# Optimization experiments

Hardware: AMD Instinct MI355X
Metric: run time of the kernel (lower is better)

Reference implementation:

```python
import jax, jax.numpy as jnp
import numpy as np

B, P, NB, WN, CI, CO = 4, 20000, 9, 17, 64, 128

def setup_inputs() -> dict:
    key = jax.random.key(0)
    k0, k1, k2, k3 = jax.random.split(key, 4)
    in_pc = jax.random.normal(k0, (B, P, CI), dtype=jnp.float32)
    raw_w_weights = jax.random.normal(k1, (P, NB, WN), dtype=jnp.float32) * 0.1
    # padded/missing neighbors use id == P, which indexes the zero-pad row and is masked
    neighbor_ids = jax.random.randint(k2, (P, NB), 0, P + 1)
    weights = jax.random.normal(k3, (WN, CO * CI), dtype=jnp.float32)
    bias = jnp.zeros((P, CO), dtype=jnp.float32)
    return {"in_pc": in_pc, "raw_w_weights": raw_w_weights, "weights": weights,
            "bias": bias, "neighbor_ids": neighbor_ids}

def reference(in_pc, raw_w_weights, weights, bias, neighbor_ids):
    b, p, ci = in_pc.shape
    wn = weights.shape[0]
    co = bias.shape[-1]
    # pc_mask: 1 for real points, 0 for the pad row (id == in_pn)
    nb_mask = (neighbor_ids < p).astype(in_pc.dtype)          # [p, nb]
    w_weights = raw_w_weights * nb_mask[:, :, None]           # [p, nb, wn]
    in_pc_pad = jnp.concatenate(
        [in_pc, jnp.zeros((b, 1, ci), dtype=in_pc.dtype)], axis=1)  # [b, p+1, ci]
    in_neighbors = in_pc_pad[:, neighbor_ids]                 # [b, p, nb, ci] gather
    # weighted fuse over neighbors into wn basis slots
    fuse = jnp.einsum('pnm,bpni->bpmi', w_weights, in_neighbors)   # [b, p, wn, ci]
    Wm = weights.reshape(wn, co, ci)
    # per-basis conv then sum-reduce over wn (b_max_pool=False), fused into one einsum
    out_pc = jnp.einsum('moi,bpmi->bpo', Wm, fuse) + bias      # [b, p, co]
    # is_final_layer=False -> ELU; residual_rate=0 -> no residual branch
    return jax.nn.elu(out_pc)
```

## Files before the change

kernel.cpp:

```cpp
#include <hip/hip_runtime.h>
#include <stdint.h>

#define B_   4
#define P_   20000
#define NB_  9
#define WN_  17
#define CI_  64
#define CO_  128
#define PTS  32
#define NBLK (P_ / PTS)

typedef __fp16 f16x8 __attribute__((ext_vector_type(8)));
typedef __fp16 h2    __attribute__((ext_vector_type(2)));
typedef float  f32x16 __attribute__((ext_vector_type(16)));

union H2U { h2 h; uint32_t u; };
union F8U { f16x8 v; h2 h[4]; uint4 u; };

__device__ __forceinline__ int b_idx(int co, int oloc) {
    int slot = (co & 1) | (((oloc ^ ((co >> 1) & 3)) & 3) << 1);
    return (co >> 1) * 64 + slot * 8;
}

__global__ void prep_wm(const float* __restrict__ w, ushort* __restrict__ wsb) {
    int i = blockIdx.x * 256 + threadIdx.x;
    int m  = i >> 10;
    int r  = i & 1023;
    int p  = r >> 9;
    int rr = r & 511;
    int co = rr >> 2, oloc = rr & 3;
    const float* src = w + (size_t)m * (CO_ * CI_) + co * CI_ + (p * 4 + oloc) * 8;
    float4 v0 = *(const float4*)(src);
    float4 v1 = *(const float4*)(src + 4);
    F8U h;
    h.h[0] = __builtin_amdgcn_cvt_pkrtz(v0.x, v0.y);
    h.h[1] = __builtin_amdgcn_cvt_pkrtz(v0.z, v0.w);
    h.h[2] = __builtin_amdgcn_cvt_pkrtz(v1.x, v1.y);
    h.h[3] = __builtin_amdgcn_cvt_pkrtz(v1.z, v1.w);
    *(uint4*)&wsb[(m * 2 + p) * 4096 + b_idx(co, oloc)] = h.u;
}

template <bool PRE>
__global__ __launch_bounds__(256, 2)
void lasm_fused(const float* __restrict__ in_pc,
                const float* __restrict__ raw_w,
                const float* __restrict__ weights,
                const float* __restrict__ bias,
                const int*   __restrict__ nbr,
                const ushort* __restrict__ wsb,
                float*       __restrict__ out)
{
    __shared__ __align__(16) int      s_nid[PTS * NB_];
    __shared__ __align__(16) uint32_t s_w2[WN_ * NB_ * 33];
    __shared__ __align__(16) ushort   s_b[2][4096];

    const int tid  = threadIdx.x;
    const int lane = tid & 63;
    const int w    = tid >> 6;
    const int arow = lane & 31;
    const int q    = lane >> 5;
    const int p0   = blockIdx.x * PTS;

    for (int t = tid; t < PTS * NB_; t += 256) s_nid[t] = nbr[p0 * NB_ + t];
    for (int idx = tid; idx < PTS * NB_ * WN_; idx += 256) {
        int pl  = idx / (NB_ * WN_);
        int rem = idx % (NB_ * WN_);
        int n   = rem / WN_;
        int m   = rem % WN_;
        float wf = raw_w[(size_t)p0 * NB_ * WN_ + idx];
        H2U c; c.h = __builtin_amdgcn_cvt_pkrtz(wf, wf);
        s_w2[(m * NB_ + n) * 33 + pl] = c.u;
    }
    __syncthreads();

    f32x16 acc[4];
    #pragma unroll
    for (int c = 0; c < 4; ++c)
        #pragma unroll
        for (int j = 0; j < 16; ++j) acc[c][j] = 0.f;

    const size_t binpc = (size_t)w * P_ * CI_;

    auto stage_b = [&](int pass, int m, int buf) {
        if (PRE) {
            #pragma unroll
            for (int j = 0; j < 2; ++j) {
                int flat = j * 256 + tid;
                uint4 v = *(const uint4*)&wsb[(size_t)(m * 2 + pass) * 4096 + flat * 8];
                *(uint4*)&s_b[buf][flat * 8] = v;
            }
        } else {
            #pragma unroll
            for (int j = 0; j < 2; ++j) {
                int flat = j * 256 + tid;
                int co = flat >> 2, oloc = flat & 3;
                const float* src = weights + (size_t)m * (CO_ * CI_) + co * CI_ + (pass * 4 + oloc) * 8;
                float4 v0 = *(const float4*)(src);
                float4 v1 = *(const float4*)(src + 4);
                F8U h;
                h.h[0] = __builtin_amdgcn_cvt_pkrtz(v0.x, v0.y);
                h.h[1] = __builtin_amdgcn_cvt_pkrtz(v0.z, v0.w);
                h.h[2] = __builtin_amdgcn_cvt_pkrtz(v1.x, v1.y);
                h.h[3] = __builtin_amdgcn_cvt_pkrtz(v1.z, v1.w);
                *(uint4*)&s_b[buf][b_idx(co, oloc)] = h.u;
            }
        }
    };

    for (int pass = 0; pass < 2; ++pass) {
        h2 x[NB_][8];
        const int ch0 = pass * 32 + q * 8;
        #pragma unroll
        for (int n = 0; n < NB_; ++n) {
            uint32_t nid = (uint32_t)s_nid[arow * NB_ + n];
            if (nid < (uint32_t)P_) {
                const float* src = in_pc + binpc + (size_t)nid * CI_ + ch0;
                float4 a0 = *(const float4*)(src);
                float4 a1 = *(const float4*)(src + 4);
                float4 b0 = *(const float4*)(src + 16);
                float4 b1 = *(const float4*)(src + 20);
                x[n][0] = __builtin_amdgcn_cvt_pkrtz(a0.x, a0.y);
                x[n][1] = __builtin_amdgcn_cvt_pkrtz(a0.z, a0.w);
                x[n][2] = __builtin_amdgcn_cvt_pkrtz(a1.x, a1.y);
                x[n][3] = __builtin_amdgcn_cvt_pkrtz(a1.z, a1.w);
                x[n][4] = __builtin_amdgcn_cvt_pkrtz(b0.x, b0.y);
                x[n][5] = __builtin_amdgcn_cvt_pkrtz(b0.z, b0.w);
                x[n][6] = __builtin_amdgcn_cvt_pkrtz(b1.x, b1.y);
                x[n][7] = __builtin_amdgcn_cvt_pkrtz(b1.z, b1.w);
            } else {
                h2 z = {(__fp16)0.f, (__fp16)0.f};
                #pragma unroll
                for (int j = 0; j < 8; ++j) x[n][j] = z;
            }
        }

        stage_b(pass, 0, 0);
        __syncthreads();

        int cur = 0;
        for (int m = 0; m < WN_; ++m) {
            int nxt = cur ^ 1;
            if (m + 1 < WN_) stage_b(pass, m + 1, nxt);

            H2U wc[9];
            #pragma unroll
            for (int n = 0; n < NB_; ++n) wc[n].u = s_w2[(m * NB_ + n) * 33 + arow];

            F8U f[2];
            #pragma unroll
            for (int kk = 0; kk < 2; ++kk) {
                #pragma unroll
                for (int r4 = 0; r4 < 4; ++r4) {
                    h2 c = {(__fp16)0.f, (__fp16)0.f};
                    #pragma unroll
                    for (int n = 0; n < NB_; ++n) c += wc[n].h * x[n][kk * 4 + r4];
                    f[kk].h[r4] = c;
                }
            }

            #pragma unroll
            for (int kk = 0; kk < 2; ++kk) {
                int oloc = kk * 2 + q;
                #pragma unroll
                for (int c = 0; c < 4; ++c) {
                    int bco = c * 32 + arow;
                    f16x8 bf = *(const f16x8*)&s_b[cur][b_idx(bco, oloc)];
                    acc[c] = __builtin_amdgcn_mfma_f32_32x32x16_f16(f[kk].v, bf, acc[c], 0, 0, 0);
                }
            }
            __syncthreads();
            cur = nxt;
        }
    }

    #pragma unroll
    for (int c = 0; c < 4; ++c) {
        int col = c * 32 + arow;
        #pragma unroll
        for (int v = 0; v < 16; ++v) {
            int lr = (v & 3) + 8 * (v >> 2) + 4 * q;
            int p  = p0 + lr;
            float val = acc[c][v] + bias[(size_t)p * CO_ + col];
            val = (val > 0.f) ? val : (__expf(val) - 1.f);
            out[((size_t)w * P_ + p) * CO_ + col] = val;
        }
    }
}

extern "C" void kernel_launch(void* const* d_in, const int* in_sizes, int n_in,
                              void* d_out, int out_size, void* d_ws, size_t ws_size,
                              hipStream_t stream) {
    const float* in_pc   = (const float*)d_in[0];
    const float* raw_w   = (const float*)d_in[1];
    const float* weights = (const float*)d_in[2];
    const float* bias    = (const float*)d_in[3];
    const int*   nbr     = (const int*)  d_in[4];
    float* out = (float*)d_out;

    const size_t need = (size_t)WN_ * 2 * 4096 * sizeof(ushort);
    if (d_ws != nullptr && ws_size >= need) {
        ushort* wsb = (ushort*)d_ws;
        prep_wm<<<dim3(WN_ * 2 * 512 / 256), dim3(256), 0, stream>>>(weights, wsb);
        lasm_fused<true><<<dim3(NBLK), dim3(256), 0, stream>>>(
            in_pc, raw_w, weights, bias, nbr, wsb, out);
    } else {
        lasm_fused<false><<<dim3(NBLK), dim3(256), 0, stream>>>(
            in_pc, raw_w, weights, bias, nbr, nullptr, out);
    }
}
```

Baseline: 171.3 us.

## Repartition block work across batch and channel halves, load weights directly from global

Halves the points per block and reassigns waves so each wave covers two batches by 16 points for half of the output channels, cutting the accumulator count. The shared-memory double-buffered weight staging and its per-basis barriers are removed; each lane now loads its weight fragments from global (L2) into registers, prefetching one step ahead. The weight prep layout is changed to match, occupancy hint raised to 3 blocks per SM, and output uses nontemporal stores. In exchange, weight fragments are fetched redundantly per wave from cache, and the blend of gathered neighbors is now recomputed by both channel-half waves.

Measured after the change: 164.1 us. -4.2%, faster.

```diff
diff --git a/kernel.cpp b/kernel.cpp
--- a/kernel.cpp
+++ b/kernel.cpp
@@ -7,7 +7,7 @@
 #define WN_  17
 #define CI_  64
 #define CO_  128
-#define PTS  32
+#define PTS  16
 #define NBLK (P_ / PTS)
 
 typedef __fp16 f16x8 __attribute__((ext_vector_type(8)));
@@ -17,18 +17,12 @@
 union H2U { h2 h; uint32_t u; };
 union F8U { f16x8 v; h2 h[4]; uint4 u; };
 
-__device__ __forceinline__ int b_idx(int co, int oloc) {
-    int slot = (co & 1) | (((oloc ^ ((co >> 1) & 3)) & 3) << 1);
-    return (co >> 1) * 64 + slot * 8;
-}
-
 __global__ void prep_wm(const float* __restrict__ w, ushort* __restrict__ wsb) {
     int i = blockIdx.x * 256 + threadIdx.x;
-    int m  = i >> 10;
-    int r  = i & 1023;
-    int p  = r >> 9;
-    int rr = r & 511;
-    int co = rr >> 2, oloc = rr & 3;
+    int m2p  = i >> 9;
+    int r    = i & 511;
+    int oloc = r >> 7, co = r & 127;
+    int m = m2p >> 1, p = m2p & 1;
     const float* src = w + (size_t)m * (CO_ * CI_) + co * CI_ + (p * 4 + oloc) * 8;
     float4 v0 = *(const float4*)(src);
     float4 v1 = *(const float4*)(src + 4);
@@ -37,11 +31,11 @@
     h.h[1] = __builtin_amdgcn_cvt_pkrtz(v0.z, v0.w);
     h.h[2] = __builtin_amdgcn_cvt_pkrtz(v1.x, v1.y);
     h.h[3] = __builtin_amdgcn_cvt_pkrtz(v1.z, v1.w);
-    *(uint4*)&wsb[(m * 2 + p) * 4096 + b_idx(co, oloc)] = h.u;
+    *(uint4*)&wsb[(size_t)((m2p * 4 + oloc) * 128 + co) * 8] = h.u;
 }
 
 template <bool PRE>
-__global__ __launch_bounds__(256, 2)
+__global__ __launch_bounds__(256, 3)
 void lasm_fused(const float* __restrict__ in_pc,
                 const float* __restrict__ raw_w,
                 const float* __restrict__ weights,
@@ -51,59 +45,57 @@
                 float*       __restrict__ out)
 {
     __shared__ __align__(16) int      s_nid[PTS * NB_];
-    __shared__ __align__(16) uint32_t s_w2[WN_ * NB_ * 33];
-    __shared__ __align__(16) ushort   s_b[2][4096];
+    __shared__ __align__(16) uint32_t s_w2[WN_ * NB_ * 17];
 
     const int tid  = threadIdx.x;
     const int lane = tid & 63;
-    const int w    = tid >> 6;
+    const int wv   = tid >> 6;
     const int arow = lane & 31;
     const int q    = lane >> 5;
+    const int mt   = wv >> 1;
+    const int ch   = wv & 1;
     const int p0   = blockIdx.x * PTS;
 
-    for (int t = tid; t < PTS * NB_; t += 256) s_nid[t] = nbr[p0 * NB_ + t];
+    if (tid < PTS * NB_) s_nid[tid] = nbr[p0 * NB_ + tid];
     for (int idx = tid; idx < PTS * NB_ * WN_; idx += 256) {
-        int pl  = idx / (NB_ * WN_);
+        int pl2 = idx / (NB_ * WN_);
         int rem = idx % (NB_ * WN_);
         int n   = rem / WN_;
         int m   = rem % WN_;
         float wf = raw_w[(size_t)p0 * NB_ * WN_ + idx];
         H2U c; c.h = __builtin_amdgcn_cvt_pkrtz(wf, wf);
-        s_w2[(m * NB_ + n) * 33 + pl] = c.u;
+        s_w2[(m * NB_ + n) * 17 + pl2] = c.u;
     }
     __syncthreads();
 
-    f32x16 acc[4];
+    f32x16 acc[2];
     #pragma unroll
-    for (int c = 0; c < 4; ++c)
+    for (int c = 0; c < 2; ++c)
         #pragma unroll
         for (int j = 0; j < 16; ++j) acc[c][j] = 0.f;
 
-    const size_t binpc = (size_t)w * P_ * CI_;
+    const int brow = mt * 2 + (arow >> 4);
+    const int pl   = arow & 15;
+    const size_t binpc = (size_t)brow * P_ * CI_;
 
-    auto stage_b = [&](int pass, int m, int buf) {
+    auto load_b = [&](int m, int pass, int kk, int c) -> f16x8 {
+        int oloc = kk * 2 + q;
         if (PRE) {
-            #pragma unroll
-            for (int j = 0; j < 2; ++j) {
-                int flat = j * 256 + tid;
-                uint4 v = *(const uint4*)&wsb[(size_t)(m * 2 + pass) * 4096 + flat * 8];
-                *(uint4*)&s_b[buf][flat * 8] = v;
-            }
+            F8U r;
+            r.u = *(const uint4*)&wsb[(size_t)(((m * 2 + pass) * 4 + oloc) * 128
+                                               + ch * 64 + c * 32 + arow) * 8];
+            return r.v;
         } else {
-            #pragma unroll
-            for (int j = 0; j < 2; ++j) {
-                int flat = j * 256 + tid;
-                int co = flat >> 2, oloc = flat & 3;
-                const float* src = weights + (size_t)m * (CO_ * CI_) + co * CI_ + (pass * 4 + oloc) * 8;
-                float4 v0 = *(const float4*)(src);
-                float4 v1 = *(const float4*)(src + 4);
-                F8U h;
-                h.h[0] = __builtin_amdgcn_cvt_pkrtz(v0.x, v0.y);
-                h.h[1] = __builtin_amdgcn_cvt_pkrtz(v0.z, v0.w);
-                h.h[2] = __builtin_amdgcn_cvt_pkrtz(v1.x, v1.y);
-                h.h[3] = __builtin_amdgcn_cvt_pkrtz(v1.z, v1.w);
-                *(uint4*)&s_b[buf][b_idx(co, oloc)] = h.u;
-            }
+            const float* s = weights + (size_t)m * (CO_ * CI_)
+                           + (ch * 64 + c * 32 + arow) * CI_ + (pass * 4 + oloc) * 8;
+            float4 v0 = *(const float4*)(s);
+            float4 v1 = *(const float4*)(s + 4);
+            F8U r;
+            r.h[0] = __builtin_amdgcn_cvt_pkrtz(v0.x, v0.y);
+            r.h[1] = __builtin_amdgcn_cvt_pkrtz(v0.z, v0.w);
+            r.h[2] = __builtin_amdgcn_cvt_pkrtz(v1.x, v1.y);
+            r.h[3] = __builtin_amdgcn_cvt_pkrtz(v1.z, v1.w);
+            return r.v;
         }
     };
 
@@ -112,7 +104,7 @@
         const int ch0 = pass * 32 + q * 8;
         #pragma unroll
         for (int n = 0; n < NB_; ++n) {
-            uint32_t nid = (uint32_t)s_nid[arow * NB_ + n];
+            uint32_t nid = (uint32_t)s_nid[pl * NB_ + n];
             if (nid < (uint32_t)P_) {
                 const float* src = in_pc + binpc + (size_t)nid * CI_ + ch0;
                 float4 a0 = *(const float4*)(src);
@@ -134,17 +126,13 @@
             }
         }
 
-        stage_b(pass, 0, 0);
-        __syncthreads();
+        f16x8 bA0 = load_b(0, pass, 0, 0);
+        f16x8 bA1 = load_b(0, pass, 0, 1);
 
-        int cur = 0;
         for (int m = 0; m < WN_; ++m) {
-            int nxt = cur ^ 1;
-            if (m + 1 < WN_) stage_b(pass, m + 1, nxt);
-
             H2U wc[9];
             #pragma unroll
-            for (int n = 0; n < NB_; ++n) wc[n].u = s_w2[(m * NB_ + n) * 33 + arow];
+            for (int n = 0; n < NB_; ++n) wc[n].u = s_w2[(m * NB_ + n) * 17 + pl];
 
             F8U f[2];
             #pragma unroll
@@ -158,31 +146,31 @@
                 }
             }
 
-            #pragma unroll
-            for (int kk = 0; kk < 2; ++kk) {
-                int oloc = kk * 2 + q;
-                #pragma unroll
-                for (int c = 0; c < 4; ++c) {
-                    int bco = c * 32 + arow;
-                    f16x8 bf = *(const f16x8*)&s_b[cur][b_idx(bco, oloc)];
-                    acc[c] = __builtin_amdgcn_mfma_f32_32x32x16_f16(f[kk].v, bf, acc[c], 0, 0, 0);
-                }
-            }
-            __syncthreads();
-            cur = nxt;
+            f16x8 bB0 = load_b(m, pass, 1, 0);
+            f16x8 bB1 = load_b(m, pass, 1, 1);
+            acc[0] = __builtin_amdgcn_mfma_f32_32x32x16_f16(f[0].v, bA0, acc[0], 0, 0, 0);
+            acc[1] = __builtin_amdgcn_mfma_f32_32x32x16_f16(f[0].v, bA1, acc[1], 0, 0, 0);
+
+            int mn = (m + 1 < WN_) ? m + 1 : m;
+            f16x8 nA0 = load_b(mn, pass, 0, 0);
+            f16x8 nA1 = load_b(mn, pass, 0, 1);
+            acc[0] = __builtin_amdgcn_mfma_f32_32x32x16_f16(f[1].v, bB0, acc[0], 0, 0, 0);
+            acc[1] = __builtin_amdgcn_mfma_f32_32x32x16_f16(f[1].v, bB1, acc[1], 0, 0, 0);
+            bA0 = nA0; bA1 = nA1;
         }
     }
 
     #pragma unroll
-    for (int c = 0; c < 4; ++c) {
-        int col = c * 32 + arow;
+    for (int c = 0; c < 2; ++c) {
+        int col = ch * 64 + c * 32 + arow;
         #pragma unroll
         for (int v = 0; v < 16; ++v) {
             int lr = (v & 3) + 8 * (v >> 2) + 4 * q;
-            int p  = p0 + lr;
+            int b  = mt * 2 + (lr >> 4);
+            int p  = p0 + (lr & 15);
             float val = acc[c][v] + bias[(size_t)p * CO_ + col];
             val = (val > 0.f) ? val : (__expf(val) - 1.f);
-            out[((size_t)w * P_ + p) * CO_ + col] = val;
+            __builtin_nontemporal_store(val, &out[((size_t)b * P_ + p) * CO_ + col]);
         }
     }
 }
```
